# Optimization experiments

Hardware: AMD Instinct MI355X
Metric: run time of the kernel (lower is better)

Reference implementation:

```python
import jax, jax.numpy as jnp
import numpy as np

B, S, D, H = 1, 4096, 1024, 16
DH = D // H

def setup_inputs() -> dict:
    key = jax.random.key(0)
    ks = jax.random.split(key, 5)
    std = float(np.sqrt(2.0 / (D + D)))
    return {
        "x": jax.random.normal(ks[0], (B, S, D), dtype=jnp.float32),
        "Wq": jax.random.normal(ks[1], (D, D), dtype=jnp.float32) * std,
        "Wk": jax.random.normal(ks[2], (D, D), dtype=jnp.float32) * std,
        "Wv": jax.random.normal(ks[3], (D, D), dtype=jnp.float32) * std,
        "Wo": jax.random.normal(ks[4], (D, D), dtype=jnp.float32) * std,
    }

def reference(x, Wq, Wk, Wv, Wo):
    # projections: input @ W.T, then split heads: b s (h d) -> b h s d
    def split_heads(t):
        b, s, _ = t.shape
        return t.reshape(b, s, H, DH).transpose(0, 2, 1, 3)
    q = split_heads(x @ Wq.T)
    k = split_heads(x @ Wk.T)
    v = split_heads(x @ Wv.T)
    scale = 1.0 / jnp.sqrt(jnp.asarray(DH, dtype=x.dtype))
    scores = jnp.einsum("bhqd,bhkd->bhqk", q, k) * scale  # (b,h,s,s)
    # causal mask: allow k <= q
    causal = jnp.tril(jnp.ones((S, S), dtype=bool))
    scores = jnp.where(causal, scores, jnp.finfo(scores.dtype).min)
    attn = jax.nn.softmax(scores, axis=-1)
    out = jnp.einsum("bhqk,bhkd->bhqd", attn, v)  # (b,h,s,d)
    out = out.transpose(0, 2, 1, 3).reshape(B, S, D)  # b h s d -> b s (h d)
    return out @ Wo.T
```

## Files before the change

kernel.cpp:

```cpp
#include <hip/hip_runtime.h>
#include <math.h>

#define SEQ 4096
#define DM  1024
#define NH  16
#define DH  64

typedef _Float16 h16;
typedef __attribute__((ext_vector_type(4))) _Float16 h16x4;
typedef __attribute__((ext_vector_type(8))) _Float16 h16x8;
typedef __attribute__((ext_vector_type(4))) float f32x4;

__global__ __launch_bounds__(256) void cvt_f32_f16(const float* __restrict__ in,
                                                   h16* __restrict__ out, int n4) {
    const int i = blockIdx.x * 256 + threadIdx.x;
    if (i < n4) {
        const float4 v = ((const float4*)in)[i];
        h16x4 o = { (h16)v.x, (h16)v.y, (h16)v.z, (h16)v.w };
        ((h16x4*)out)[i] = o;
    }
}

#define GST 40

template<int OUT>
__global__ __launch_bounds__(256) void gemm_mfma(const h16* __restrict__ A,
                                                 const h16* __restrict__ B,
                                                 void* __restrict__ Cv,
                                                 int M, int N, int K) {
    __shared__ h16 As[128 * GST];
    __shared__ h16 Bs[128 * GST];

    const int t    = threadIdx.x;
    const int lane = t & 63;
    const int w    = t >> 6;
    const int wm   = (w >> 1) * 64;
    const int wn   = (w & 1) * 64;
    const int l15  = lane & 15;
    const int lq8  = (lane >> 4) * 8;
    const int m0   = blockIdx.y * 128;
    const int n0   = blockIdx.x * 128;

    const int lrow = t >> 2;
    const int lcol = (t & 3) * 8;

    f32x4 acc[4][4] = {};

    const h16* pA0 = A + (size_t)(m0 + lrow) * K + lcol;
    const h16* pA1 = A + (size_t)(m0 + 64 + lrow) * K + lcol;
    const h16* pB0 = B + (size_t)(n0 + lrow) * K + lcol;
    const h16* pB1 = B + (size_t)(n0 + 64 + lrow) * K + lcol;

    h16x8 ra0 = *(const h16x8*)pA0;
    h16x8 ra1 = *(const h16x8*)pA1;
    h16x8 rb0 = *(const h16x8*)pB0;
    h16x8 rb1 = *(const h16x8*)pB1;

    for (int k0 = 0; k0 < K; k0 += 32) {
        __syncthreads();
        *(h16x8*)&As[lrow * GST + lcol]        = ra0;
        *(h16x8*)&As[(64 + lrow) * GST + lcol] = ra1;
        *(h16x8*)&Bs[lrow * GST + lcol]        = rb0;
        *(h16x8*)&Bs[(64 + lrow) * GST + lcol] = rb1;
        __syncthreads();
        if (k0 + 32 < K) {
            ra0 = *(const h16x8*)(pA0 + k0 + 32);
            ra1 = *(const h16x8*)(pA1 + k0 + 32);
            rb0 = *(const h16x8*)(pB0 + k0 + 32);
            rb1 = *(const h16x8*)(pB1 + k0 + 32);
        }
        h16x8 af[4], bf[4];
        #pragma unroll
        for (int i = 0; i < 4; ++i)
            af[i] = *(const h16x8*)&As[(wm + i * 16 + l15) * GST + lq8];
        #pragma unroll
        for (int j = 0; j < 4; ++j)
            bf[j] = *(const h16x8*)&Bs[(wn + j * 16 + l15) * GST + lq8];
        #pragma unroll
        for (int i = 0; i < 4; ++i)
            #pragma unroll
            for (int j = 0; j < 4; ++j)
                acc[i][j] = __builtin_amdgcn_mfma_f32_16x16x32_f16(af[i], bf[j], acc[i][j], 0, 0, 0);
    }

    const int cr = wm + (lane >> 4) * 4;
    const int cc = wn + l15;
    #pragma unroll
    for (int i = 0; i < 4; ++i)
        #pragma unroll
        for (int j = 0; j < 4; ++j)
            #pragma unroll
            for (int r = 0; r < 4; ++r) {
                const int gm = m0 + cr + i * 16 + r;
                const int gn = n0 + cc + j * 16;
                if (OUT == 2)      ((float*)Cv)[(size_t)gm * N + gn] = acc[i][j][r];
                else if (OUT == 0) ((h16*)Cv)[(size_t)gm * N + gn] = (h16)acc[i][j][r];
                else               ((h16*)Cv)[(size_t)gn * M + gm] = (h16)acc[i][j][r];
            }
}

#define AST 80

__device__ __forceinline__ void tile_softmax(const f32x4 s[4], float& m_st, float& l_st,
                                             f32x4 o[4], h16* ps_row, bool diag,
                                             int q_loc, int lq) {
    float sv[4][4];
    float mx = m_st;
    #pragma unroll
    for (int jj = 0; jj < 4; ++jj)
        #pragma unroll
        for (int r = 0; r < 4; ++r) {
            float x = s[jj][r] * 0.125f;
            if (diag && (jj * 16 + lq * 4 + r) > q_loc) x = -1e30f;
            sv[jj][r] = x;
            mx = fmaxf(mx, x);
        }
    mx = fmaxf(mx, __shfl_xor(mx, 16, 64));
    mx = fmaxf(mx, __shfl_xor(mx, 32, 64));
    const float alpha = __expf(m_st - mx);
    m_st = mx;
    float sum = 0.0f;
    #pragma unroll
    for (int jj = 0; jj < 4; ++jj) {
        const float p0 = __expf(sv[jj][0] - mx);
        const float p1 = __expf(sv[jj][1] - mx);
        const float p2 = __expf(sv[jj][2] - mx);
        const float p3 = __expf(sv[jj][3] - mx);
        sum += (p0 + p1) + (p2 + p3);
        h16x4 pk = { (h16)p0, (h16)p1, (h16)p2, (h16)p3 };
        *(h16x4*)(ps_row + jj * 16 + lq * 4) = pk;
    }
    sum += __shfl_xor(sum, 16, 64);
    sum += __shfl_xor(sum, 32, 64);
    l_st = l_st * alpha + sum;
    #pragma unroll
    for (int jj = 0; jj < 4; ++jj)
        #pragma unroll
        for (int r = 0; r < 4; ++r)
            o[jj][r] *= alpha;
}

__global__ __launch_bounds__(256, 2) void flash_attn_mfma(
        const h16* __restrict__ Qg, const h16* __restrict__ Kg,
        const h16* __restrict__ Vt, h16* __restrict__ Og) {
    __shared__ h16 Ks[2][64 * AST];
    __shared__ h16 Vs[2][64 * AST];
    __shared__ h16 Ps[128 * AST];

    const int qA   = blockIdx.x;
    const int qB   = 63 - qA;
    const int hh   = blockIdx.y;
    const int t    = threadIdx.x;
    const int lane = t & 63;
    const int w    = t >> 6;
    const int l15  = lane & 15;
    const int lq   = lane >> 4;
    const int lq8  = lq * 8;
    const int hc   = hh * DH;
    const int q_loc = w * 16 + l15;

    const int r1 = t >> 3;
    const int r2 = r1 + 32;
    const int c1 = (t & 7) * 8;

    {
        const int qa0 = qA * 64, qb0 = qB * 64;
        *(h16x8*)&Ks[0][r1 * AST + c1] = *(const h16x8*)(Qg + (size_t)(qa0 + r1) * DM + hc + c1);
        *(h16x8*)&Ks[0][r2 * AST + c1] = *(const h16x8*)(Qg + (size_t)(qa0 + r2) * DM + hc + c1);
        *(h16x8*)&Vs[0][r1 * AST + c1] = *(const h16x8*)(Qg + (size_t)(qb0 + r1) * DM + hc + c1);
        *(h16x8*)&Vs[0][r2 * AST + c1] = *(const h16x8*)(Qg + (size_t)(qb0 + r2) * DM + hc + c1);
    }
    h16x8 kv1 = *(const h16x8*)(Kg + (size_t)(r1) * DM + hc + c1);
    h16x8 kv2 = *(const h16x8*)(Kg + (size_t)(r2) * DM + hc + c1);
    h16x8 vv1 = *(const h16x8*)(Vt + (size_t)(hc + r1) * SEQ + c1);
    h16x8 vv2 = *(const h16x8*)(Vt + (size_t)(hc + r2) * SEQ + c1);

    __syncthreads();
    h16x8 qfA[2], qfB[2];
    qfA[0] = *(const h16x8*)&Ks[0][q_loc * AST + lq8];
    qfA[1] = *(const h16x8*)&Ks[0][q_loc * AST + 32 + lq8];
    qfB[0] = *(const h16x8*)&Vs[0][q_loc * AST + lq8];
    qfB[1] = *(const h16x8*)&Vs[0][q_loc * AST + 32 + lq8];
    __syncthreads();

    float mA = -1e30f, lA = 0.0f, mB = -1e30f, lB = 0.0f;
    f32x4 oA[4] = {}, oB[4] = {};
    h16* const psA = &Ps[(size_t)q_loc * AST];
    h16* const psB = &Ps[(size_t)(64 + q_loc) * AST];

    for (int kt = 0; kt <= qB; ++kt) {
        h16* const Ksb = &Ks[kt & 1][0];
        h16* const Vsb = &Vs[kt & 1][0];
        *(h16x8*)&Ksb[r1 * AST + c1] = kv1;
        *(h16x8*)&Ksb[r2 * AST + c1] = kv2;
        *(h16x8*)&Vsb[r1 * AST + c1] = vv1;
        *(h16x8*)&Vsb[r2 * AST + c1] = vv2;
        __syncthreads();
        if (kt < qB) {
            const int k0n = (kt + 1) * 64;
            kv1 = *(const h16x8*)(Kg + (size_t)(k0n + r1) * DM + hc + c1);
            kv2 = *(const h16x8*)(Kg + (size_t)(k0n + r2) * DM + hc + c1);
            vv1 = *(const h16x8*)(Vt + (size_t)(hc + r1) * SEQ + k0n + c1);
            vv2 = *(const h16x8*)(Vt + (size_t)(hc + r2) * SEQ + k0n + c1);
        }
        const bool doA = (kt <= qA);

        f32x4 sA[4] = {}, sB[4] = {};
        #pragma unroll
        for (int kc = 0; kc < 2; ++kc)
            #pragma unroll
            for (int jj = 0; jj < 4; ++jj) {
                const h16x8 kf = *(const h16x8*)&Ksb[(jj * 16 + l15) * AST + kc * 32 + lq8];
                if (doA) sA[jj] = __builtin_amdgcn_mfma_f32_16x16x32_f16(kf, qfA[kc], sA[jj], 0, 0, 0);
                sB[jj] = __builtin_amdgcn_mfma_f32_16x16x32_f16(kf, qfB[kc], sB[jj], 0, 0, 0);
            }

        if (doA) tile_softmax(sA, mA, lA, oA, psA, kt == qA, q_loc, lq);
        tile_softmax(sB, mB, lB, oB, psB, kt == qB, q_loc, lq);

        asm volatile("s_waitcnt lgkmcnt(0)" ::: "memory");
        h16x8 pfA[2], pfB[2];
        if (doA) {
            pfA[0] = *(const h16x8*)(psA + lq8);
            pfA[1] = *(const h16x8*)(psA + 32 + lq8);
        }
        pfB[0] = *(const h16x8*)(psB + lq8);
        pfB[1] = *(const h16x8*)(psB + 32 + lq8);

        #pragma unroll
        for (int kc = 0; kc < 2; ++kc)
            #pragma unroll
            for (int jj = 0; jj < 4; ++jj) {
                const h16x8 vf = *(const h16x8*)&Vsb[(jj * 16 + l15) * AST + kc * 32 + lq8];
                if (doA) oA[jj] = __builtin_amdgcn_mfma_f32_16x16x32_f16(vf, pfA[kc], oA[jj], 0, 0, 0);
                oB[jj] = __builtin_amdgcn_mfma_f32_16x16x32_f16(vf, pfB[kc], oB[jj], 0, 0, 0);
            }
    }

    {
        const float il = 1.0f / lA;
        const size_t qg = (size_t)(qA * 64 + q_loc) * DM + hc;
        #pragma unroll
        for (int jj = 0; jj < 4; ++jj) {
            h16x4 ov = { (h16)(oA[jj][0] * il), (h16)(oA[jj][1] * il),
                         (h16)(oA[jj][2] * il), (h16)(oA[jj][3] * il) };
            *(h16x4*)(Og + qg + jj * 16 + lq * 4) = ov;
        }
    }
    {
        const float il = 1.0f / lB;
        const size_t qg = (size_t)(qB * 64 + q_loc) * DM + hc;
        #pragma unroll
        for (int jj = 0; jj < 4; ++jj) {
            h16x4 ov = { (h16)(oB[jj][0] * il), (h16)(oB[jj][1] * il),
                         (h16)(oB[jj][2] * il), (h16)(oB[jj][3] * il) };
            *(h16x4*)(Og + qg + jj * 16 + lq * 4) = ov;
        }
    }
}

extern "C" void kernel_launch(void* const* d_in, const int* in_sizes, int n_in,
                              void* d_out, int out_size, void* d_ws, size_t ws_size,
                              hipStream_t stream) {
    const float* x  = (const float*)d_in[0];
    const float* Wq = (const float*)d_in[1];
    const float* Wk = (const float*)d_in[2];
    const float* Wv = (const float*)d_in[3];
    const float* Wo = (const float*)d_in[4];
    float* out = (float*)d_out;

    const size_t SD = (size_t)SEQ * DM;
    const size_t DD = (size_t)DM * DM;

    h16* xh  = (h16*)d_ws;
    h16* wqh = xh + SD;
    h16* wkh = wqh + DD;
    h16* wvh = wkh + DD;
    h16* woh = wvh + DD;
    h16* Qh  = woh + DD;
    h16* Kh  = Qh + SD;
    h16* Vth = Kh + SD;
    h16* AOh = Vth + SD;

    cvt_f32_f16<<<(int)(SD / 4 / 256), 256, 0, stream>>>(x,  xh,  (int)(SD / 4));
    cvt_f32_f16<<<(int)(DD / 4 / 256), 256, 0, stream>>>(Wq, wqh, (int)(DD / 4));
    cvt_f32_f16<<<(int)(DD / 4 / 256), 256, 0, stream>>>(Wk, wkh, (int)(DD / 4));
    cvt_f32_f16<<<(int)(DD / 4 / 256), 256, 0, stream>>>(Wv, wvh, (int)(DD / 4));
    cvt_f32_f16<<<(int)(DD / 4 / 256), 256, 0, stream>>>(Wo, woh, (int)(DD / 4));

    const dim3 blk(256);
    const dim3 gg(DM / 128, SEQ / 128);

    gemm_mfma<0><<<gg, blk, 0, stream>>>(xh, wqh, Qh,  SEQ, DM, DM);
    gemm_mfma<0><<<gg, blk, 0, stream>>>(xh, wkh, Kh,  SEQ, DM, DM);
    gemm_mfma<1><<<gg, blk, 0, stream>>>(xh, wvh, Vth, SEQ, DM, DM);

    flash_attn_mfma<<<dim3(32, NH), blk, 0, stream>>>(Qh, Kh, Vth, AOh);

    gemm_mfma<2><<<gg, blk, 0, stream>>>(AOh, woh, out, SEQ, DM, DM);
}
```

Baseline: 276.0 us.

## Fuse fp32-to-fp16 conversion into GEMM loads and fold softmax scale into Q

```diff
diff --git a/kernel.cpp b/kernel.cpp
--- a/kernel.cpp
+++ b/kernel.cpp
@@ -11,121 +11,154 @@
 typedef __attribute__((ext_vector_type(8))) _Float16 h16x8;
 typedef __attribute__((ext_vector_type(4))) float f32x4;
 
-__global__ __launch_bounds__(256) void cvt_f32_f16(const float* __restrict__ in,
-                                                   h16* __restrict__ out, int n4) {
-    const int i = blockIdx.x * 256 + threadIdx.x;
-    if (i < n4) {
-        const float4 v = ((const float4*)in)[i];
-        h16x4 o = { (h16)v.x, (h16)v.y, (h16)v.z, (h16)v.w };
-        ((h16x4*)out)[i] = o;
-    }
+__device__ __forceinline__ h16x4 cvt4(f32x4 v) {
+    h16x4 o = { (h16)v.x, (h16)v.y, (h16)v.z, (h16)v.w };
+    return o;
 }
 
 #define GST 40
 
-template<int OUT>
-__global__ __launch_bounds__(256) void gemm_mfma(const h16* __restrict__ A,
-                                                 const h16* __restrict__ B,
-                                                 void* __restrict__ Cv,
-                                                 int M, int N, int K) {
-    __shared__ h16 As[128 * GST];
-    __shared__ h16 Bs[128 * GST];
+template<int OUT, int AF32>
+__global__ __launch_bounds__(256, 2) void gemm_mfma(const void* __restrict__ Av,
+                                                    const float* __restrict__ B,
+                                                    void* __restrict__ Cv,
+                                                    int M, int N, int K, float escale) {
+    __shared__ h16 As[2][64 * GST];
+    __shared__ h16 Bs[2][128 * GST];
 
     const int t    = threadIdx.x;
     const int lane = t & 63;
     const int w    = t >> 6;
-    const int wm   = (w >> 1) * 64;
+    const int wm   = (w >> 1) * 32;
     const int wn   = (w & 1) * 64;
     const int l15  = lane & 15;
-    const int lq8  = (lane >> 4) * 8;
-    const int m0   = blockIdx.y * 128;
+    const int lq   = lane >> 4;
+    const int lq8  = lq * 8;
+    const int m0   = blockIdx.y * 64;
     const int n0   = blockIdx.x * 128;
 
-    const int lrow = t >> 2;
-    const int lcol = (t & 3) * 8;
-
-    f32x4 acc[4][4] = {};
-
-    const h16* pA0 = A + (size_t)(m0 + lrow) * K + lcol;
-    const h16* pA1 = A + (size_t)(m0 + 64 + lrow) * K + lcol;
-    const h16* pB0 = B + (size_t)(n0 + lrow) * K + lcol;
-    const h16* pB1 = B + (size_t)(n0 + 64 + lrow) * K + lcol;
-
-    h16x8 ra0 = *(const h16x8*)pA0;
-    h16x8 ra1 = *(const h16x8*)pA1;
-    h16x8 rb0 = *(const h16x8*)pB0;
-    h16x8 rb1 = *(const h16x8*)pB1;
-
+    const int srow = t >> 3;
+    const int sc4  = (t & 7) * 4;
+    const int arow = t >> 2;
+    const int ac8  = (t & 3) * 8;
+
+    const float* Af = (const float*)Av;
+    const h16*   Ah = (const h16*)Av;
+
+    f32x4 acc[2][4] = {};
+
+    f32x4 a0[2], a1[2], b0[4], b1[4];
+    h16x8 ha0, ha1;
+
+    if (AF32) {
+        a0[0] = *(const f32x4*)(Af + (size_t)(m0 + srow) * K + sc4);
+        a0[1] = *(const f32x4*)(Af + (size_t)(m0 + 32 + srow) * K + sc4);
+        a1[0] = *(const f32x4*)(Af + (size_t)(m0 + srow) * K + 32 + sc4);
+        a1[1] = *(const f32x4*)(Af + (size_t)(m0 + 32 + srow) * K + 32 + sc4);
+    } else {
+        ha0 = *(const h16x8*)(Ah + (size_t)(m0 + arow) * K + ac8);
+        ha1 = *(const h16x8*)(Ah + (size_t)(m0 + arow) * K + 32 + ac8);
+    }
+    #pragma unroll
+    for (int c = 0; c < 4; ++c) {
+        b0[c] = *(const f32x4*)(B + (size_t)(n0 + srow + 32 * c) * K + sc4);
+        b1[c] = *(const f32x4*)(B + (size_t)(n0 + srow + 32 * c) * K + 32 + sc4);
+    }
+
+    int p = 0;
     for (int k0 = 0; k0 < K; k0 += 32) {
+        if (AF32) {
+            *(h16x4*)&As[p][srow * GST + sc4]        = cvt4(a0[0]);
+            *(h16x4*)&As[p][(32 + srow) * GST + sc4] = cvt4(a0[1]);
+        } else {
+            *(h16x8*)&As[p][arow * GST + ac8] = ha0;
+        }
+        #pragma unroll
+        for (int c = 0; c < 4; ++c)
+            *(h16x4*)&Bs[p][(srow + 32 * c) * GST + sc4] = cvt4(b0[c]);
         __syncthreads();
-        *(h16x8*)&As[lrow * GST + lcol]        = ra0;
-        *(h16x8*)&As[(64 + lrow) * GST + lcol] = ra1;
-        *(h16x8*)&Bs[lrow * GST + lcol]        = rb0;
-        *(h16x8*)&Bs[(64 + lrow) * GST + lcol] = rb1;
-        __syncthreads();
-        if (k0 + 32 < K) {
-            ra0 = *(const h16x8*)(pA0 + k0 + 32);
-            ra1 = *(const h16x8*)(pA1 + k0 + 32);
-            rb0 = *(const h16x8*)(pB0 + k0 + 32);
-            rb1 = *(const h16x8*)(pB1 + k0 + 32);
-        }
-        h16x8 af[4], bf[4];
-        #pragma unroll
-        for (int i = 0; i < 4; ++i)
-            af[i] = *(const h16x8*)&As[(wm + i * 16 + l15) * GST + lq8];
+
+        if (AF32) { a0[0] = a1[0]; a0[1] = a1[1]; } else { ha0 = ha1; }
+        #pragma unroll
+        for (int c = 0; c < 4; ++c) b0[c] = b1[c];
+        if (k0 + 64 < K) {
+            if (AF32) {
+                a1[0] = *(const f32x4*)(Af + (size_t)(m0 + srow) * K + k0 + 64 + sc4);
+                a1[1] = *(const f32x4*)(Af + (size_t)(m0 + 32 + srow) * K + k0 + 64 + sc4);
+            } else {
+                ha1 = *(const h16x8*)(Ah + (size_t)(m0 + arow) * K + k0 + 64 + ac8);
+            }
+            #pragma unroll
+            for (int c = 0; c < 4; ++c)
+                b1[c] = *(const f32x4*)(B + (size_t)(n0 + srow + 32 * c) * K + k0 + 64 + sc4);
+        }
+
+        h16x8 af[2], bf[4];
+        #pragma unroll
+        for (int i = 0; i < 2; ++i)
+            af[i] = *(const h16x8*)&As[p][(wm + i * 16 + l15) * GST + lq8];
         #pragma unroll
         for (int j = 0; j < 4; ++j)
-            bf[j] = *(const h16x8*)&Bs[(wn + j * 16 + l15) * GST + lq8];
-        #pragma unroll
-        for (int i = 0; i < 4; ++i)
+            bf[j] = *(const h16x8*)&Bs[p][(wn + j * 16 + l15) * GST + lq8];
+        #pragma unroll
+        for (int i = 0; i < 2; ++i)
             #pragma unroll
             for (int j = 0; j < 4; ++j)
                 acc[i][j] = __builtin_amdgcn_mfma_f32_16x16x32_f16(af[i], bf[j], acc[i][j], 0, 0, 0);
-    }
-
-    const int cr = wm + (lane >> 4) * 4;
+        p ^= 1;
+    }
+
+    const int cr = wm + lq * 4;
     const int cc = wn + l15;
     #pragma unroll
-    for (int i = 0; i < 4; ++i)
-        #pragma unroll
-        for (int j = 0; j < 4; ++j)
-            #pragma unroll
-            for (int r = 0; r < 4; ++r) {
-                const int gm = m0 + cr + i * 16 + r;
-                const int gn = n0 + cc + j * 16;
-                if (OUT == 2)      ((float*)Cv)[(size_t)gm * N + gn] = acc[i][j][r];
-                else if (OUT == 0) ((h16*)Cv)[(size_t)gm * N + gn] = (h16)acc[i][j][r];
-                else               ((h16*)Cv)[(size_t)gn * M + gm] = (h16)acc[i][j][r];
+    for (int i = 0; i < 2; ++i)
+        #pragma unroll
+        for (int j = 0; j < 4; ++j) {
+            const int gm0 = m0 + cr + i * 16;
+            const int gn  = n0 + cc + j * 16;
+            if (OUT == 1) {
+                h16x4 v = { (h16)(acc[i][j][0] * escale), (h16)(acc[i][j][1] * escale),
+                            (h16)(acc[i][j][2] * escale), (h16)(acc[i][j][3] * escale) };
+                *(h16x4*)((h16*)Cv + (size_t)gn * M + gm0) = v;
+            } else {
+                #pragma unroll
+                for (int r = 0; r < 4; ++r) {
+                    if (OUT == 2) ((float*)Cv)[(size_t)(gm0 + r) * N + gn] = acc[i][j][r] * escale;
+                    else          ((h16*)Cv)[(size_t)(gm0 + r) * N + gn] = (h16)(acc[i][j][r] * escale);
+                }
             }
-}
-
-#define AST 80
-
-__device__ __forceinline__ void tile_softmax(const f32x4 s[4], float& m_st, float& l_st,
+        }
+}
+
+#define AST 72
+
+__device__ __forceinline__ void tile_softmax(f32x4 s[4], float& m_st, float& l_st,
                                              f32x4 o[4], h16* ps_row, bool diag,
                                              int q_loc, int lq) {
-    float sv[4][4];
+    if (diag) {
+        #pragma unroll
+        for (int jj = 0; jj < 4; ++jj)
+            #pragma unroll
+            for (int r = 0; r < 4; ++r)
+                if ((jj * 16 + lq * 4 + r) > q_loc) s[jj][r] = -1e30f;
+    }
     float mx = m_st;
     #pragma unroll
     for (int jj = 0; jj < 4; ++jj)
         #pragma unroll
-        for (int r = 0; r < 4; ++r) {
-            float x = s[jj][r] * 0.125f;
-            if (diag && (jj * 16 + lq * 4 + r) > q_loc) x = -1e30f;
-            sv[jj][r] = x;
-            mx = fmaxf(mx, x);
-        }
+        for (int r = 0; r < 4; ++r)
+            mx = fmaxf(mx, s[jj][r]);
     mx = fmaxf(mx, __shfl_xor(mx, 16, 64));
     mx = fmaxf(mx, __shfl_xor(mx, 32, 64));
-    const float alpha = __expf(m_st - mx);
+    const float alpha = exp2f(m_st - mx);
     m_st = mx;
     float sum = 0.0f;
     #pragma unroll
     for (int jj = 0; jj < 4; ++jj) {
-        const float p0 = __expf(sv[jj][0] - mx);
-        const float p1 = __expf(sv[jj][1] - mx);
-        const float p2 = __expf(sv[jj][2] - mx);
-        const float p3 = __expf(sv[jj][3] - mx);
+        const float p0 = exp2f(s[jj][0] - mx);
+        const float p1 = exp2f(s[jj][1] - mx);
+        const float p2 = exp2f(s[jj][2] - mx);
+        const float p3 = exp2f(s[jj][3] - mx);
         sum += (p0 + p1) + (p2 + p3);
         h16x4 pk = { (h16)p0, (h16)p1, (h16)p2, (h16)p3 };
         *(h16x4*)(ps_row + jj * 16 + lq * 4) = pk;
@@ -140,12 +173,12 @@
             o[jj][r] *= alpha;
 }
 
-__global__ __launch_bounds__(256, 2) void flash_attn_mfma(
+__global__ __launch_bounds__(256, 4) void flash_attn_mfma(
         const h16* __restrict__ Qg, const h16* __restrict__ Kg,
         const h16* __restrict__ Vt, h16* __restrict__ Og) {
-    __shared__ h16 Ks[2][64 * AST];
-    __shared__ h16 Vs[2][64 * AST];
-    __shared__ h16 Ps[128 * AST];
+    __shared__ h16 Ks[64 * AST];
+    __shared__ h16 Vs[64 * AST];
+    __shared__ h16 Ps[2][64 * AST];
 
     const int qA   = blockIdx.x;
     const int qB   = 63 - qA;
@@ -165,10 +198,10 @@
 
     {
         const int qa0 = qA * 64, qb0 = qB * 64;
-        *(h16x8*)&Ks[0][r1 * AST + c1] = *(const h16x8*)(Qg + (size_t)(qa0 + r1) * DM + hc + c1);
-        *(h16x8*)&Ks[0][r2 * AST + c1] = *(const h16x8*)(Qg + (size_t)(qa0 + r2) * DM + hc + c1);
-        *(h16x8*)&Vs[0][r1 * AST + c1] = *(const h16x8*)(Qg + (size_t)(qb0 + r1) * DM + hc + c1);
-        *(h16x8*)&Vs[0][r2 * AST + c1] = *(const h16x8*)(Qg + (size_t)(qb0 + r2) * DM + hc + c1);
+        *(h16x8*)&Ks[r1 * AST + c1] = *(const h16x8*)(Qg + (size_t)(qa0 + r1) * DM + hc + c1);
+        *(h16x8*)&Ks[r2 * AST + c1] = *(const h16x8*)(Qg + (size_t)(qa0 + r2) * DM + hc + c1);
+        *(h16x8*)&Vs[r1 * AST + c1] = *(const h16x8*)(Qg + (size_t)(qb0 + r1) * DM + hc + c1);
+        *(h16x8*)&Vs[r2 * AST + c1] = *(const h16x8*)(Qg + (size_t)(qb0 + r2) * DM + hc + c1);
     }
     h16x8 kv1 = *(const h16x8*)(Kg + (size_t)(r1) * DM + hc + c1);
     h16x8 kv2 = *(const h16x8*)(Kg + (size_t)(r2) * DM + hc + c1);
@@ -177,24 +210,22 @@
 
     __syncthreads();
     h16x8 qfA[2], qfB[2];
-    qfA[0] = *(const h16x8*)&Ks[0][q_loc * AST + lq8];
-    qfA[1] = *(const h16x8*)&Ks[0][q_loc * AST + 32 + lq8];
-    qfB[0] = *(const h16x8*)&Vs[0][q_loc * AST + lq8];
-    qfB[1] = *(const h16x8*)&Vs[0][q_loc * AST + 32 + lq8];
-    __syncthreads();
+    qfA[0] = *(const h16x8*)&Ks[q_loc * AST + lq8];
+    qfA[1] = *(const h16x8*)&Ks[q_loc * AST + 32 + lq8];
+    qfB[0] = *(const h16x8*)&Vs[q_loc * AST + lq8];
+    qfB[1] = *(const h16x8*)&Vs[q_loc * AST + 32 + lq8];
 
     float mA = -1e30f, lA = 0.0f, mB = -1e30f, lB = 0.0f;
     f32x4 oA[4] = {}, oB[4] = {};
-    h16* const psA = &Ps[(size_t)q_loc * AST];
-    h16* const psB = &Ps[(size_t)(64 + q_loc) * AST];
+    h16* const psA = &Ps[0][(size_t)q_loc * AST];
+    h16* const psB = &Ps[1][(size_t)q_loc * AST];
 
     for (int kt = 0; kt <= qB; ++kt) {
-        h16* const Ksb = &Ks[kt & 1][0];
-        h16* const Vsb = &Vs[kt & 1][0];
-        *(h16x8*)&Ksb[r1 * AST + c1] = kv1;
-        *(h16x8*)&Ksb[r2 * AST + c1] = kv2;
-        *(h16x8*)&Vsb[r1 * AST + c1] = vv1;
-        *(h16x8*)&Vsb[r2 * AST + c1] = vv2;
+        __syncthreads();
+        *(h16x8*)&Ks[r1 * AST + c1] = kv1;
+        *(h16x8*)&Ks[r2 * AST + c1] = kv2;
+        *(h16x8*)&Vs[r1 * AST + c1] = vv1;
+        *(h16x8*)&Vs[r2 * AST + c1] = vv2;
         __syncthreads();
         if (kt < qB) {
             const int k0n = (kt + 1) * 64;
@@ -210,7 +241,7 @@
         for (int kc = 0; kc < 2; ++kc)
             #pragma unroll
             for (int jj = 0; jj < 4; ++jj) {
-                const h16x8 kf = *(const h16x8*)&Ksb[(jj * 16 + l15) * AST + kc * 32 + lq8];
+                const h16x8 kf = *(const h16x8*)&Ks[(jj * 16 + l15) * AST + kc * 32 + lq8];
                 if (doA) sA[jj] = __builtin_amdgcn_mfma_f32_16x16x32_f16(kf, qfA[kc], sA[jj], 0, 0, 0);
                 sB[jj] = __builtin_amdgcn_mfma_f32_16x16x32_f16(kf, qfB[kc], sB[jj], 0, 0, 0);
             }
@@ -231,7 +262,7 @@
         for (int kc = 0; kc < 2; ++kc)
             #pragma unroll
             for (int jj = 0; jj < 4; ++jj) {
-                const h16x8 vf = *(const h16x8*)&Vsb[(jj * 16 + l15) * AST + kc * 32 + lq8];
+                const h16x8 vf = *(const h16x8*)&Vs[(jj * 16 + l15) * AST + kc * 32 + lq8];
                 if (doA) oA[jj] = __builtin_amdgcn_mfma_f32_16x16x32_f16(vf, pfA[kc], oA[jj], 0, 0, 0);
                 oB[jj] = __builtin_amdgcn_mfma_f32_16x16x32_f16(vf, pfB[kc], oB[jj], 0, 0, 0);
             }
@@ -270,32 +301,22 @@
     float* out = (float*)d_out;
 
     const size_t SD = (size_t)SEQ * DM;
-    const size_t DD = (size_t)DM * DM;
-
-    h16* xh  = (h16*)d_ws;
-    h16* wqh = xh + SD;
-    h16* wkh = wqh + DD;
-    h16* wvh = wkh + DD;
-    h16* woh = wvh + DD;
-    h16* Qh  = woh + DD;
+
+    h16* Qh  = (h16*)d_ws;
     h16* Kh  = Qh + SD;
     h16* Vth = Kh + SD;
     h16* AOh = Vth + SD;
 
-    cvt_f32_f16<<<(int)(SD / 4 / 256), 256, 0, stream>>>(x,  xh,  (int)(SD / 4));
-    cvt_f32_f16<<<(int)(DD / 4 / 256), 256, 0, stream>>>(Wq, wqh, (int)(DD / 4));
-    cvt_f32_f16<<<(int)(DD / 4 / 256), 256, 0, stream>>>(Wk, wkh, (int)(DD / 4));
-    cvt_f32_f16<<<(int)(DD / 4 / 256), 256, 0, stream>>>(Wv, wvh, (int)(DD / 4));
-    cvt_f32_f16<<<(int)(DD / 4 / 256), 256, 0, stream>>>(Wo, woh, (int)(DD / 4));
-
     const dim3 blk(256);
-    const dim3 gg(DM / 128, SEQ / 128);
-
-    gemm_mfma<0><<<gg, blk, 0, stream>>>(xh, wqh, Qh,  SEQ, DM, DM);
-    gemm_mfma<0><<<gg, blk, 0, stream>>>(xh, wkh, Kh,  SEQ, DM, DM);
-    gemm_mfma<1><<<gg, blk, 0, stream>>>(xh, wvh, Vth, SEQ, DM, DM);
+    const dim3 gg(DM / 128, SEQ / 64);
+
+    const float SCL = 0.125f * 1.44269504088896340736f;
+
+    gemm_mfma<0, 1><<<gg, blk, 0, stream>>>(x, Wq, Qh,  SEQ, DM, DM, SCL);
+    gemm_mfma<0, 1><<<gg, blk, 0, stream>>>(x, Wk, Kh,  SEQ, DM, DM, 1.0f);
+    gemm_mfma<1, 1><<<gg, blk, 0, stream>>>(x, Wv, Vth, SEQ, DM, DM, 1.0f);
 
     flash_attn_mfma<<<dim3(32, NH), blk, 0, stream>>>(Qh, Kh, Vth, AOh);
 
-    gemm_mfma<2><<<gg, blk, 0, stream>>>(AOh, woh, out, SEQ, DM, DM);
-}
+    gemm_mfma<2, 0><<<gg, blk, 0, stream>>>(AOh, Wo, out, SEQ, DM, DM, 1.0f);
+}
```

After: 583.3 us. 2.11x slower.

## Fuse QKV GEMMs, halve GEMM tiles, fold softmax scale into Q, exp2

Applied to the files above, without the earlier changes.

```diff
diff --git a/kernel.cpp b/kernel.cpp
--- a/kernel.cpp
+++ b/kernel.cpp
@@ -23,109 +23,194 @@
 
 #define GST 40
 
-template<int OUT>
-__global__ __launch_bounds__(256) void gemm_mfma(const h16* __restrict__ A,
-                                                 const h16* __restrict__ B,
-                                                 void* __restrict__ Cv,
-                                                 int M, int N, int K) {
-    __shared__ h16 As[128 * GST];
-    __shared__ h16 Bs[128 * GST];
-
+__global__ __launch_bounds__(256, 2) void gemm_qkv(const h16* __restrict__ xh,
+                                                   const h16* __restrict__ Wq,
+                                                   const h16* __restrict__ Wk,
+                                                   const h16* __restrict__ Wv,
+                                                   h16* __restrict__ Qh,
+                                                   h16* __restrict__ Kh,
+                                                   h16* __restrict__ Vth,
+                                                   float scl) {
+    __shared__ h16 As[2][64 * GST];
+    __shared__ h16 Bs[2][128 * GST];
+
+    const int z    = blockIdx.z;
+    const h16* B   = (z == 0) ? Wq : (z == 1) ? Wk : Wv;
     const int t    = threadIdx.x;
     const int lane = t & 63;
     const int w    = t >> 6;
-    const int wm   = (w >> 1) * 64;
+    const int wm   = (w >> 1) * 32;
     const int wn   = (w & 1) * 64;
     const int l15  = lane & 15;
-    const int lq8  = (lane >> 4) * 8;
-    const int m0   = blockIdx.y * 128;
+    const int lq   = lane >> 4;
+    const int lq8  = lq * 8;
+    const int m0   = blockIdx.y * 64;
     const int n0   = blockIdx.x * 128;
-
-    const int lrow = t >> 2;
-    const int lcol = (t & 3) * 8;
-
-    f32x4 acc[4][4] = {};
-
-    const h16* pA0 = A + (size_t)(m0 + lrow) * K + lcol;
-    const h16* pA1 = A + (size_t)(m0 + 64 + lrow) * K + lcol;
-    const h16* pB0 = B + (size_t)(n0 + lrow) * K + lcol;
-    const h16* pB1 = B + (size_t)(n0 + 64 + lrow) * K + lcol;
-
-    h16x8 ra0 = *(const h16x8*)pA0;
-    h16x8 ra1 = *(const h16x8*)pA1;
+    const int K    = DM, M = SEQ, N = DM;
+
+    const int arow = t >> 2;
+    const int ac8  = (t & 3) * 8;
+
+    f32x4 acc[2][4] = {};
+
+    const h16* pA  = xh + (size_t)(m0 + arow) * K + ac8;
+    const h16* pB0 = B + (size_t)(n0 + arow) * K + ac8;
+    const h16* pB1 = B + (size_t)(n0 + 64 + arow) * K + ac8;
+
+    h16x8 ra = *(const h16x8*)pA;
     h16x8 rb0 = *(const h16x8*)pB0;
     h16x8 rb1 = *(const h16x8*)pB1;
 
     for (int k0 = 0; k0 < K; k0 += 32) {
-        __syncthreads();
-        *(h16x8*)&As[lrow * GST + lcol]        = ra0;
-        *(h16x8*)&As[(64 + lrow) * GST + lcol] = ra1;
-        *(h16x8*)&Bs[lrow * GST + lcol]        = rb0;
-        *(h16x8*)&Bs[(64 + lrow) * GST + lcol] = rb1;
+        const int p = (k0 >> 5) & 1;
+        *(h16x8*)&As[p][arow * GST + ac8]        = ra;
+        *(h16x8*)&Bs[p][arow * GST + ac8]        = rb0;
+        *(h16x8*)&Bs[p][(64 + arow) * GST + ac8] = rb1;
         __syncthreads();
         if (k0 + 32 < K) {
-            ra0 = *(const h16x8*)(pA0 + k0 + 32);
-            ra1 = *(const h16x8*)(pA1 + k0 + 32);
+            ra  = *(const h16x8*)(pA + k0 + 32);
             rb0 = *(const h16x8*)(pB0 + k0 + 32);
             rb1 = *(const h16x8*)(pB1 + k0 + 32);
         }
-        h16x8 af[4], bf[4];
-        #pragma unroll
-        for (int i = 0; i < 4; ++i)
-            af[i] = *(const h16x8*)&As[(wm + i * 16 + l15) * GST + lq8];
+        h16x8 af[2], bf[4];
+        #pragma unroll
+        for (int i = 0; i < 2; ++i)
+            af[i] = *(const h16x8*)&As[p][(wm + i * 16 + l15) * GST + lq8];
         #pragma unroll
         for (int j = 0; j < 4; ++j)
-            bf[j] = *(const h16x8*)&Bs[(wn + j * 16 + l15) * GST + lq8];
-        #pragma unroll
-        for (int i = 0; i < 4; ++i)
+            bf[j] = *(const h16x8*)&Bs[p][(wn + j * 16 + l15) * GST + lq8];
+        #pragma unroll
+        for (int i = 0; i < 2; ++i)
             #pragma unroll
             for (int j = 0; j < 4; ++j)
                 acc[i][j] = __builtin_amdgcn_mfma_f32_16x16x32_f16(af[i], bf[j], acc[i][j], 0, 0, 0);
     }
 
-    const int cr = wm + (lane >> 4) * 4;
+    const int cr = wm + lq * 4;
+    const int cc = wn + l15;
+    if (z == 2) {
+        #pragma unroll
+        for (int i = 0; i < 2; ++i)
+            #pragma unroll
+            for (int j = 0; j < 4; ++j) {
+                const int gm0 = m0 + cr + i * 16;
+                const int gn  = n0 + cc + j * 16;
+                h16x4 v = { (h16)acc[i][j][0], (h16)acc[i][j][1],
+                            (h16)acc[i][j][2], (h16)acc[i][j][3] };
+                *(h16x4*)(Vth + (size_t)gn * M + gm0) = v;
+            }
+    } else {
+        h16* Og = (z == 0) ? Qh : Kh;
+        const float e = (z == 0) ? scl : 1.0f;
+        #pragma unroll
+        for (int i = 0; i < 2; ++i)
+            #pragma unroll
+            for (int j = 0; j < 4; ++j)
+                #pragma unroll
+                for (int r = 0; r < 4; ++r) {
+                    const int gm = m0 + cr + i * 16 + r;
+                    const int gn = n0 + cc + j * 16;
+                    Og[(size_t)gm * N + gn] = (h16)(acc[i][j][r] * e);
+                }
+    }
+}
+
+__global__ __launch_bounds__(256, 2) void gemm_out(const h16* __restrict__ A,
+                                                   const h16* __restrict__ B,
+                                                   float* __restrict__ C) {
+    __shared__ h16 As[2][64 * GST];
+    __shared__ h16 Bs[2][128 * GST];
+
+    const int t    = threadIdx.x;
+    const int lane = t & 63;
+    const int w    = t >> 6;
+    const int wm   = (w >> 1) * 32;
+    const int wn   = (w & 1) * 64;
+    const int l15  = lane & 15;
+    const int lq   = lane >> 4;
+    const int lq8  = lq * 8;
+    const int m0   = blockIdx.y * 64;
+    const int n0   = blockIdx.x * 128;
+    const int K    = DM, N = DM;
+
+    const int arow = t >> 2;
+    const int ac8  = (t & 3) * 8;
+
+    f32x4 acc[2][4] = {};
+
+    const h16* pA  = A + (size_t)(m0 + arow) * K + ac8;
+    const h16* pB0 = B + (size_t)(n0 + arow) * K + ac8;
+    const h16* pB1 = B + (size_t)(n0 + 64 + arow) * K + ac8;
+
+    h16x8 ra = *(const h16x8*)pA;
+    h16x8 rb0 = *(const h16x8*)pB0;
+    h16x8 rb1 = *(const h16x8*)pB1;
+
+    for (int k0 = 0; k0 < K; k0 += 32) {
+        const int p = (k0 >> 5) & 1;
+        *(h16x8*)&As[p][arow * GST + ac8]        = ra;
+        *(h16x8*)&Bs[p][arow * GST + ac8]        = rb0;
+        *(h16x8*)&Bs[p][(64 + arow) * GST + ac8] = rb1;
+        __syncthreads();
+        if (k0 + 32 < K) {
+            ra  = *(const h16x8*)(pA + k0 + 32);
+            rb0 = *(const h16x8*)(pB0 + k0 + 32);
+            rb1 = *(const h16x8*)(pB1 + k0 + 32);
+        }
+        h16x8 af[2], bf[4];
+        #pragma unroll
+        for (int i = 0; i < 2; ++i)
+            af[i] = *(const h16x8*)&As[p][(wm + i * 16 + l15) * GST + lq8];
+        #pragma unroll
+        for (int j = 0; j < 4; ++j)
+            bf[j] = *(const h16x8*)&Bs[p][(wn + j * 16 + l15) * GST + lq8];
+        #pragma unroll
+        for (int i = 0; i < 2; ++i)
+            #pragma unroll
+            for (int j = 0; j < 4; ++j)
+                acc[i][j] = __builtin_amdgcn_mfma_f32_16x16x32_f16(af[i], bf[j], acc[i][j], 0, 0, 0);
+    }
+
+    const int cr = wm + lq * 4;
     const int cc = wn + l15;
     #pragma unroll
-    for (int i = 0; i < 4; ++i)
+    for (int i = 0; i < 2; ++i)
         #pragma unroll
         for (int j = 0; j < 4; ++j)
             #pragma unroll
-            for (int r = 0; r < 4; ++r) {
-                const int gm = m0 + cr + i * 16 + r;
-                const int gn = n0 + cc + j * 16;
-                if (OUT == 2)      ((float*)Cv)[(size_t)gm * N + gn] = acc[i][j][r];
-                else if (OUT == 0) ((h16*)Cv)[(size_t)gm * N + gn] = (h16)acc[i][j][r];
-                else               ((h16*)Cv)[(size_t)gn * M + gm] = (h16)acc[i][j][r];
-            }
-}
-
-#define AST 80
-
-__device__ __forceinline__ void tile_softmax(const f32x4 s[4], float& m_st, float& l_st,
+            for (int r = 0; r < 4; ++r)
+                C[(size_t)(m0 + cr + i * 16 + r) * N + n0 + cc + j * 16] = acc[i][j][r];
+}
+
+#define AST 72
+
+__device__ __forceinline__ void tile_softmax(f32x4 s[4], float& m_st, float& l_st,
                                              f32x4 o[4], h16* ps_row, bool diag,
                                              int q_loc, int lq) {
-    float sv[4][4];
+    if (diag) {
+        #pragma unroll
+        for (int jj = 0; jj < 4; ++jj)
+            #pragma unroll
+            for (int r = 0; r < 4; ++r)
+                if ((jj * 16 + lq * 4 + r) > q_loc) s[jj][r] = -1e30f;
+    }
     float mx = m_st;
     #pragma unroll
     for (int jj = 0; jj < 4; ++jj)
         #pragma unroll
-        for (int r = 0; r < 4; ++r) {
-            float x = s[jj][r] * 0.125f;
-            if (diag && (jj * 16 + lq * 4 + r) > q_loc) x = -1e30f;
-            sv[jj][r] = x;
-            mx = fmaxf(mx, x);
-        }
+        for (int r = 0; r < 4; ++r)
+            mx = fmaxf(mx, s[jj][r]);
     mx = fmaxf(mx, __shfl_xor(mx, 16, 64));
     mx = fmaxf(mx, __shfl_xor(mx, 32, 64));
-    const float alpha = __expf(m_st - mx);
+    const float alpha = exp2f(m_st - mx);
     m_st = mx;
     float sum = 0.0f;
     #pragma unroll
     for (int jj = 0; jj < 4; ++jj) {
-        const float p0 = __expf(sv[jj][0] - mx);
-        const float p1 = __expf(sv[jj][1] - mx);
-        const float p2 = __expf(sv[jj][2] - mx);
-        const float p3 = __expf(sv[jj][3] - mx);
+        const float p0 = exp2f(s[jj][0] - mx);
+        const float p1 = exp2f(s[jj][1] - mx);
+        const float p2 = exp2f(s[jj][2] - mx);
+        const float p3 = exp2f(s[jj][3] - mx);
         sum += (p0 + p1) + (p2 + p3);
         h16x4 pk = { (h16)p0, (h16)p1, (h16)p2, (h16)p3 };
         *(h16x4*)(ps_row + jj * 16 + lq * 4) = pk;
@@ -145,7 +230,7 @@
         const h16* __restrict__ Vt, h16* __restrict__ Og) {
     __shared__ h16 Ks[2][64 * AST];
     __shared__ h16 Vs[2][64 * AST];
-    __shared__ h16 Ps[128 * AST];
+    __shared__ h16 Ps[2][64 * AST];
 
     const int qA   = blockIdx.x;
     const int qB   = 63 - qA;
@@ -185,8 +270,8 @@
 
     float mA = -1e30f, lA = 0.0f, mB = -1e30f, lB = 0.0f;
     f32x4 oA[4] = {}, oB[4] = {};
-    h16* const psA = &Ps[(size_t)q_loc * AST];
-    h16* const psB = &Ps[(size_t)(64 + q_loc) * AST];
+    h16* const psA = &Ps[0][(size_t)q_loc * AST];
+    h16* const psB = &Ps[1][(size_t)q_loc * AST];
 
     for (int kt = 0; kt <= qB; ++kt) {
         h16* const Ksb = &Ks[kt & 1][0];
@@ -289,13 +374,13 @@
     cvt_f32_f16<<<(int)(DD / 4 / 256), 256, 0, stream>>>(Wo, woh, (int)(DD / 4));
 
     const dim3 blk(256);
-    const dim3 gg(DM / 128, SEQ / 128);
-
-    gemm_mfma<0><<<gg, blk, 0, stream>>>(xh, wqh, Qh,  SEQ, DM, DM);
-    gemm_mfma<0><<<gg, blk, 0, stream>>>(xh, wkh, Kh,  SEQ, DM, DM);
-    gemm_mfma<1><<<gg, blk, 0, stream>>>(xh, wvh, Vth, SEQ, DM, DM);
+
+    const float SCL = 0.125f * 1.44269504088896340736f;
+
+    gemm_qkv<<<dim3(DM / 128, SEQ / 64, 3), blk, 0, stream>>>(
+        xh, wqh, wkh, wvh, Qh, Kh, Vth, SCL);
 
     flash_attn_mfma<<<dim3(32, NH), blk, 0, stream>>>(Qh, Kh, Vth, AOh);
 
-    gemm_mfma<2><<<gg, blk, 0, stream>>>(AOh, woh, out, SEQ, DM, DM);
-}
+    gemm_out<<<dim3(DM / 128, SEQ / 64), blk, 0, stream>>>(AOh, woh, out);
+}
```

Result: faster. 263.5 us (-4.5%).
